# Kernel tuning notes

Measured on AMD Instinct MI355X. Metric: run time of the kernel, lower is better.

Reference implementation:

```python
import jax, jax.numpy as jnp
import numpy as np

B, T, D, H = 8, 1024, 1024, 16
HD = D // H  # 64
FF = 4 * D


def setup_inputs() -> dict:
    key = jax.random.key(0)
    ks = jax.random.split(key, 16)
    s = lambda k, shape, scale: (jax.random.normal(k, shape, dtype=jnp.float32) * scale)
    return {
        "x": s(ks[0], (B, T, D), 1.0),
        "ln1_g": jnp.ones((D,), jnp.float32),
        "ln1_b": jnp.zeros((D,), jnp.float32),
        "ln2_g": jnp.ones((D,), jnp.float32),
        "ln2_b": jnp.zeros((D,), jnp.float32),
        "Wq": s(ks[1], (H, D, HD), 0.02), "bq": jnp.zeros((H, HD), jnp.float32),
        "Wk": s(ks[2], (H, D, HD), 0.02), "bk": jnp.zeros((H, HD), jnp.float32),
        "Wv": s(ks[3], (H, D, HD), 0.02), "bv": jnp.zeros((H, HD), jnp.float32),
        "Wo": s(ks[4], (D, D), 0.02), "bo": jnp.zeros((D,), jnp.float32),
        "W1": s(ks[5], (D, FF), 0.02), "b1": jnp.zeros((FF,), jnp.float32),
        "W2": s(ks[6], (FF, D), 0.02), "b2": jnp.zeros((D,), jnp.float32),
    }


def layer_norm(x, g, b, eps=1e-5):
    mu = jnp.mean(x, axis=-1, keepdims=True)
    var = jnp.mean(jnp.square(x - mu), axis=-1, keepdims=True)
    return (x - mu) * jax.lax.rsqrt(var + eps) * g + b


def reference(x, ln1_g, ln1_b, ln2_g, ln2_b, Wq, bq, Wk, bk, Wv, bv, Wo, bo, W1, b1, W2, b2):
    h = layer_norm(x, ln1_g, ln1_b)
    # Per-head Q/K/V projections, batched over heads (equivalent to the
    # Python loop of per-head Linears in the original module).
    q = jnp.einsum("btd,hde->bhte", h, Wq) + bq[None, :, None, :]
    k = jnp.einsum("btd,hde->bhte", h, Wk) + bk[None, :, None, :]
    v = jnp.einsum("btd,hde->bhte", h, Wv) + bv[None, :, None, :]
    scores = jnp.einsum("bhte,bhse->bhts", q, k) / jnp.sqrt(jnp.float32(HD))
    att = jax.nn.softmax(scores, axis=-1)  # no causal mask in source
    ctx = jnp.einsum("bhts,bhse->bhte", att, v)
    # concat heads along feature dim
    ctx = jnp.transpose(ctx, (0, 2, 1, 3)).reshape(B, T, D)
    attn_out = ctx @ Wo + bo
    x = x + attn_out
    h2 = layer_norm(x, ln2_g, ln2_b)
    ff = jax.nn.gelu(h2 @ W1 + b1, approximate=False) @ W2 + b2
    return x + ff
```

## Files before the change

### kernel.cpp

```cpp
#include <hip/hip_runtime.h>
#include <hip/hip_bf16.h>
#include <cstdint>
#include <cstddef>


typedef __bf16 bf16;
typedef __bf16 bf16x8 __attribute__((ext_vector_type(8)));
typedef __bf16 bf16x4 __attribute__((ext_vector_type(4)));
typedef float  f32x4  __attribute__((ext_vector_type(4)));

#define BB    8
#define TT    1024
#define DD    1024
#define HH    16
#define HDIM  64
#define FFD   4096
#define MROWS (BB*TT)

__device__ __forceinline__ void async_ld16(const void* g, void* l) {
  __builtin_amdgcn_global_load_lds(
      (const __attribute__((address_space(1))) uint32_t*)g,
      (__attribute__((address_space(3))) uint32_t*)l, 16, 0, 0);
}

__global__ void k_transpose_cast(const float* __restrict__ src, bf16* __restrict__ dst,
                                 int K, int N) {
  __shared__ float tile[32][33];
  const size_t boff = (size_t)blockIdx.z * K * N;
  src += boff; dst += boff;
  const int k0 = blockIdx.y * 32, n0 = blockIdx.x * 32;
  const int tx = threadIdx.x, ty = threadIdx.y;
#pragma unroll
  for (int i = 0; i < 4; ++i)
    tile[ty + i*8][tx] = src[(size_t)(k0 + ty + i*8) * N + n0 + tx];
  __syncthreads();
#pragma unroll
  for (int i = 0; i < 4; ++i)
    dst[(size_t)(n0 + ty + i*8) * K + k0 + tx] = (bf16)tile[tx][ty + i*8];
}

__global__ void k_concat_bias(const float* __restrict__ bq, const float* __restrict__ bk,
                              const float* __restrict__ bv, float* __restrict__ out) {
  int i = blockIdx.x * 256 + threadIdx.x;
  float v = (i < 1024) ? bq[i] : (i < 2048) ? bk[i - 1024] : bv[i - 2048];
  out[i] = v;
}

__global__ void k_transpose_v(const bf16* __restrict__ qkv, bf16* __restrict__ vT) {
  __shared__ bf16 tile[32][33];
  const int bh = blockIdx.z;
  const int b = bh >> 4, h = bh & 15;
  const int t0 = blockIdx.x * 32, e0 = blockIdx.y * 32;
  const int tx = threadIdx.x, ty = threadIdx.y;
  const bf16* src = qkv + (size_t)b * TT * 3072 + 2048 + h * 64;
#pragma unroll
  for (int i = 0; i < 4; ++i)
    tile[ty + i*8][tx] = src[(size_t)(t0 + ty + i*8) * 3072 + e0 + tx];
  __syncthreads();
  bf16* dst = vT + ((size_t)bh * 64 + e0) * TT + t0;
#pragma unroll
  for (int i = 0; i < 4; ++i)
    dst[(size_t)(ty + i*8) * TT + tx] = tile[tx][ty + i*8];
}

__global__ void k_layernorm(const float* __restrict__ x, const float* __restrict__ g,
                            const float* __restrict__ b, bf16* __restrict__ out) {
  const int row = blockIdx.x, tid = threadIdx.x;
  const float* xr = x + (size_t)row * DD;
  f32x4 v = *(const f32x4*)(xr + tid * 4);
  float s  = v[0] + v[1] + v[2] + v[3];
  float ss = v[0]*v[0] + v[1]*v[1] + v[2]*v[2] + v[3]*v[3];
#pragma unroll
  for (int m = 1; m < 64; m <<= 1) { s += __shfl_xor(s, m); ss += __shfl_xor(ss, m); }
  __shared__ float red[8];
  const int wid = tid >> 6;
  if ((tid & 63) == 0) { red[wid*2] = s; red[wid*2+1] = ss; }
  __syncthreads();
  s  = red[0] + red[2] + red[4] + red[6];
  ss = red[1] + red[3] + red[5] + red[7];
  const float mu = s * (1.0f / DD);
  const float var = ss * (1.0f / DD) - mu * mu;
  const float rs = rsqrtf(var + 1e-5f);
  bf16x4 o;
#pragma unroll
  for (int j = 0; j < 4; ++j)
    o[j] = (bf16)((v[j] - mu) * rs * g[tid*4 + j] + b[tid*4 + j]);
  *(bf16x4*)&out[(size_t)row * DD + tid * 4] = o;
}

template<int MODE>
__global__ __launch_bounds__(512, 2)
void k_gemm256(const bf16* __restrict__ A, const bf16* __restrict__ Bt,
               const float* __restrict__ bias, bf16* __restrict__ outb,
               int M, int N, int K) {
  __shared__ __align__(16) bf16 As[2][256 * 64];
  __shared__ __align__(16) bf16 Bs[2][256 * 64];
  const int tid = threadIdx.x;
  const int w = tid >> 6, l = tid & 63;
  const int wm = w >> 2, wn = w & 3;
  const int l15 = l & 15, l4 = l >> 4;

  const int nbx = N >> 8;
  const int nwg = gridDim.x;
  const int cpx = nwg >> 3;
  const int swz = (blockIdx.x & 7) * cpx + (blockIdx.x >> 3);
  const int m0 = (swz / nbx) << 8, n0 = (swz % nbx) << 8;

  f32x4 acc[8][4] = {};

  const int srow = l >> 3;
  const int sch = l & 7;

  const int NT = K >> 6;

#define STAGE_A(buf, kt, rb) { \
    const int r_ = (rb) + w*8 + srow; \
    const int ch_ = sch ^ (r_ & 7); \
    async_ld16(A + (size_t)(m0 + r_) * K + (kt)*64 + ch_*8, &As[buf][((rb) + w*8)*64]); }
#define STAGE_B(buf, kt, rb) { \
    const int r_ = (rb) + w*8 + srow; \
    const int ch_ = sch ^ (r_ & 7); \
    async_ld16(Bt + (size_t)(n0 + r_) * K + (kt)*64 + ch_*8, &Bs[buf][((rb) + w*8)*64]); }

  STAGE_A(0, 0, 0)   STAGE_A(0, 0, 64)  STAGE_A(0, 0, 128) STAGE_A(0, 0, 192)
  STAGE_B(0, 0, 0)   STAGE_B(0, 0, 64)  STAGE_B(0, 0, 128) STAGE_B(0, 0, 192)
  STAGE_A(1, 1, 0)   STAGE_A(1, 1, 64)  STAGE_A(1, 1, 128) STAGE_A(1, 1, 192)
  asm volatile("s_waitcnt vmcnt(4)" ::: "memory");
  __builtin_amdgcn_sched_barrier(0);
  __builtin_amdgcn_s_barrier();

  for (int t = 0; t < NT; ++t) {
    const int p = t & 1;
    bf16x8 a0[8], b0[4], a1[8], b1[4];

#pragma unroll
    for (int mf = 0; mf < 8; ++mf) {
      const int row = wm*128 + mf*16 + l15;
      const int ch = l4 ^ (row & 7);
      a0[mf] = *(const bf16x8*)&As[p][row*64 + ch*8];
    }
#pragma unroll
    for (int nf = 0; nf < 4; ++nf) {
      const int row = wn*64 + nf*16 + l15;
      const int ch = l4 ^ (row & 7);
      b0[nf] = *(const bf16x8*)&Bs[p][row*64 + ch*8];
    }
    if (t + 1 < NT) { STAGE_B(p^1, t+1, 0) STAGE_B(p^1, t+1, 64) }
    __builtin_amdgcn_s_barrier();
    asm volatile("s_waitcnt lgkmcnt(0)" ::: "memory");
    __builtin_amdgcn_sched_barrier(0);
    __builtin_amdgcn_s_setprio(1);
#pragma unroll
    for (int mf = 0; mf < 4; ++mf)
#pragma unroll
      for (int nf = 0; nf < 4; ++nf)
        acc[mf][nf] = __builtin_amdgcn_mfma_f32_16x16x32_bf16(a0[mf], b0[nf], acc[mf][nf], 0, 0, 0);
    __builtin_amdgcn_s_setprio(0);
    __builtin_amdgcn_s_barrier();

#pragma unroll
    for (int mf = 0; mf < 8; ++mf) {
      const int row = wm*128 + mf*16 + l15;
      const int ch = (4 + l4) ^ (row & 7);
      a1[mf] = *(const bf16x8*)&As[p][row*64 + ch*8];
    }
#pragma unroll
    for (int nf = 0; nf < 4; ++nf) {
      const int row = wn*64 + nf*16 + l15;
      const int ch = (4 + l4) ^ (row & 7);
      b1[nf] = *(const bf16x8*)&Bs[p][row*64 + ch*8];
    }
    if (t + 1 < NT) { STAGE_B(p^1, t+1, 128) STAGE_B(p^1, t+1, 192) }
    __builtin_amdgcn_s_barrier();
    asm volatile("s_waitcnt lgkmcnt(0)" ::: "memory");
    __builtin_amdgcn_sched_barrier(0);
    __builtin_amdgcn_s_setprio(1);
#pragma unroll
    for (int mf = 4; mf < 8; ++mf)
#pragma unroll
      for (int nf = 0; nf < 4; ++nf)
        acc[mf][nf] = __builtin_amdgcn_mfma_f32_16x16x32_bf16(a0[mf], b0[nf], acc[mf][nf], 0, 0, 0);
    __builtin_amdgcn_s_setprio(0);
    __builtin_amdgcn_s_barrier();

    if (t + 2 < NT) { STAGE_A(p, t+2, 0) STAGE_A(p, t+2, 64) }
    __builtin_amdgcn_s_barrier();
    __builtin_amdgcn_s_setprio(1);
#pragma unroll
    for (int mf = 0; mf < 4; ++mf)
#pragma unroll
      for (int nf = 0; nf < 4; ++nf)
        acc[mf][nf] = __builtin_amdgcn_mfma_f32_16x16x32_bf16(a1[mf], b1[nf], acc[mf][nf], 0, 0, 0);
    __builtin_amdgcn_s_setprio(0);
    __builtin_amdgcn_s_barrier();

    if (t + 2 < NT) { STAGE_A(p, t+2, 128) STAGE_A(p, t+2, 192) }
    __builtin_amdgcn_s_barrier();
    __builtin_amdgcn_s_setprio(1);
#pragma unroll
    for (int mf = 4; mf < 8; ++mf)
#pragma unroll
      for (int nf = 0; nf < 4; ++nf)
        acc[mf][nf] = __builtin_amdgcn_mfma_f32_16x16x32_bf16(a1[mf], b1[nf], acc[mf][nf], 0, 0, 0);
    __builtin_amdgcn_s_setprio(0);
    if (t < NT - 2) { asm volatile("s_waitcnt vmcnt(4)" ::: "memory"); }
    else            { asm volatile("s_waitcnt vmcnt(0)" ::: "memory"); }
    __builtin_amdgcn_sched_barrier(0);
    __builtin_amdgcn_s_barrier();
  }
#undef STAGE_A
#undef STAGE_B

#pragma unroll
  for (int mf = 0; mf < 8; ++mf) {
#pragma unroll
    for (int r = 0; r < 4; ++r) {
      const size_t grow = (size_t)(m0 + wm*128 + mf*16 + l4*4 + r);
      const size_t rowoff = grow * (size_t)N;
#pragma unroll
      for (int nf = 0; nf < 4; ++nf) {
        const int gcol = n0 + wn*64 + nf*16 + l15;
        float v = acc[mf][nf][r] + bias[gcol];
        if constexpr (MODE == 1)
          v = 0.5f * v * (1.0f + erff(v * 0.70710678118654752440f));
        outb[rowoff + gcol] = (bf16)v;
      }
    }
  }
}

template<int MODE>
__global__ __launch_bounds__(256)
void k_gemm(const bf16* __restrict__ A, const bf16* __restrict__ Bt,
            const float* __restrict__ bias, const float* __restrict__ res,
            bf16* __restrict__ outb, float* __restrict__ outf,
            int M, int N, int K) {
  __shared__ __align__(16) bf16 As[128 * 64];
  __shared__ __align__(16) bf16 Bs[128 * 64];
  const int tid = threadIdx.x;
  const int w = tid >> 6, l = tid & 63;
  const int wm = w >> 1, wn = w & 1;
  const int l15 = l & 15, l4 = l >> 4;
  const int m0 = blockIdx.y * 128, n0 = blockIdx.x * 128;

  f32x4 acc[4][4] = {};

  const int srow0 = w * 32 + (l >> 3);
  const int sl7 = l & 7;

  for (int k0 = 0; k0 < K; k0 += 64) {
#pragma unroll
    for (int j = 0; j < 4; ++j) {
      const int row = srow0 + j * 8;
      const int ch = sl7 ^ (row & 7);
      async_ld16(A + (size_t)(m0 + row) * K + k0 + ch * 8, &As[(w*32 + j*8) * 64]);
    }
#pragma unroll
    for (int j = 0; j < 4; ++j) {
      const int row = srow0 + j * 8;
      const int ch = sl7 ^ (row & 7);
      async_ld16(Bt + (size_t)(n0 + row) * K + k0 + ch * 8, &Bs[(w*32 + j*8) * 64]);
    }
    __syncthreads();
#pragma unroll
    for (int kk = 0; kk < 2; ++kk) {
      bf16x8 af[4], bfr[4];
#pragma unroll
      for (int mf = 0; mf < 4; ++mf) {
        const int row = wm*64 + mf*16 + l15;
        const int ch = (kk*4 + l4) ^ (row & 7);
        af[mf] = *(const bf16x8*)&As[row*64 + ch*8];
      }
#pragma unroll
      for (int nf = 0; nf < 4; ++nf) {
        const int row = wn*64 + nf*16 + l15;
        const int ch = (kk*4 + l4) ^ (row & 7);
        bfr[nf] = *(const bf16x8*)&Bs[row*64 + ch*8];
      }
#pragma unroll
      for (int mf = 0; mf < 4; ++mf)
#pragma unroll
        for (int nf = 0; nf < 4; ++nf)
          acc[mf][nf] = __builtin_amdgcn_mfma_f32_16x16x32_bf16(af[mf], bfr[nf], acc[mf][nf], 0, 0, 0);
    }
    __syncthreads();
  }

#pragma unroll
  for (int mf = 0; mf < 4; ++mf) {
#pragma unroll
    for (int r = 0; r < 4; ++r) {
      const size_t grow = (size_t)(m0 + wm*64 + mf*16 + l4*4 + r);
      const size_t rowoff = grow * (size_t)N;
#pragma unroll
      for (int nf = 0; nf < 4; ++nf) {
        const int gcol = n0 + wn*64 + nf*16 + l15;
        float v = acc[mf][nf][r] + bias[gcol];
        if constexpr (MODE == 1)
          v = 0.5f * v * (1.0f + erff(v * 0.70710678118654752440f));
        if constexpr (MODE == 2) {
          v += res[rowoff + gcol];
          outf[rowoff + gcol] = v;
        } else {
          outb[rowoff + gcol] = (bf16)v;
        }
      }
    }
  }
}

__global__ __launch_bounds__(256)
void k_attn(const bf16* __restrict__ qkv, const bf16* __restrict__ vT,
            bf16* __restrict__ ctx) {
  const int qt = blockIdx.x, h = blockIdx.y, b = blockIdx.z;
  const int tid = threadIdx.x;
  const int w = tid >> 6, l = tid & 63;
  const int l15 = l & 15, l4 = l >> 4;

  __shared__ __align__(16) bf16 Ks[2][64 * 64];
  __shared__ __align__(16) bf16 Vs[2][64 * 64];
  __shared__ __align__(16) bf16 P[4][16][72];

  const bf16* base = qkv + (size_t)b * TT * 3072;
  const bf16* Qp = base + h * 64;
  const bf16* Kp = base + 1024 + h * 64;
  const bf16* Vtp = vT + ((size_t)(b * HH + h)) * HDIM * TT;

  const int qrow = qt * 64 + w * 16 + l15;
  bf16x8 qf[2];
  qf[0] = *(const bf16x8*)&Qp[(size_t)qrow * 3072 + l4 * 8];
  qf[1] = *(const bf16x8*)&Qp[(size_t)qrow * 3072 + 32 + l4 * 8];

  f32x4 oacc[4] = {};
  float mrow[4] = {-1e30f, -1e30f, -1e30f, -1e30f};
  float lrow[4] = {0.f, 0.f, 0.f, 0.f};

  const int sr = (l >> 3);
  const int sl7 = l & 7;

  auto stage = [&](int buf, int t) {
    const int kv0 = t * 64;
#pragma unroll
    for (int j = 0; j < 2; ++j) {
      const int row = w*16 + j*8 + sr;
      const int ch = sl7 ^ (row & 7);
      async_ld16(Kp + (size_t)(kv0 + row) * 3072 + ch * 8, &Ks[buf][(w*16 + j*8) * 64]);
    }
#pragma unroll
    for (int j = 0; j < 2; ++j) {
      const int row = w*16 + j*8 + sr;
      const int ch = sl7 ^ (row & 7);
      async_ld16(Vtp + (size_t)row * TT + kv0 + ch * 8, &Vs[buf][(w*16 + j*8) * 64]);
    }
  };

  stage(0, 0);
  for (int t = 0; t < TT / 64; ++t) {
    const int cur = t & 1;
    __syncthreads();
    if (t + 1 < TT / 64) stage(cur ^ 1, t + 1);

    f32x4 sacc[4] = {};
#pragma unroll
    for (int nf = 0; nf < 4; ++nf) {
      const int row = nf*16 + l15;
#pragma unroll
      for (int kk = 0; kk < 2; ++kk) {
        const int ch = (kk*4 + l4) ^ (row & 7);
        bf16x8 kfr = *(const bf16x8*)&Ks[cur][row*64 + ch*8];
        sacc[nf] = __builtin_amdgcn_mfma_f32_16x16x32_bf16(qf[kk], kfr, sacc[nf], 0, 0, 0);
      }
    }
    float mnew[4], ef[4];
#pragma unroll
    for (int r = 0; r < 4; ++r) {
      float mx = -1e30f;
#pragma unroll
      for (int nf = 0; nf < 4; ++nf) { sacc[nf][r] *= 0.125f; mx = fmaxf(mx, sacc[nf][r]); }
      mx = fmaxf(mx, __shfl_xor(mx, 1));
      mx = fmaxf(mx, __shfl_xor(mx, 2));
      mx = fmaxf(mx, __shfl_xor(mx, 4));
      mx = fmaxf(mx, __shfl_xor(mx, 8));
      mnew[r] = fmaxf(mrow[r], mx);
      ef[r] = __expf(mrow[r] - mnew[r]);
      mrow[r] = mnew[r];
    }
#pragma unroll
    for (int r = 0; r < 4; ++r) {
      float rs = 0.f;
#pragma unroll
      for (int nf = 0; nf < 4; ++nf) {
        const float p = __expf(sacc[nf][r] - mnew[r]);
        rs += p;
        P[w][l4*4 + r][l15 + nf*16] = (bf16)p;
      }
      rs += __shfl_xor(rs, 1); rs += __shfl_xor(rs, 2);
      rs += __shfl_xor(rs, 4); rs += __shfl_xor(rs, 8);
      lrow[r] = lrow[r] * ef[r] + rs;
#pragma unroll
      for (int nf = 0; nf < 4; ++nf) oacc[nf][r] *= ef[r];
    }
#pragma unroll
    for (int kk = 0; kk < 2; ++kk) {
      bf16x8 pa = *(const bf16x8*)&P[w][l15][kk*32 + l4*8];
#pragma unroll
      for (int nf = 0; nf < 4; ++nf) {
        const int row = nf*16 + l15;
        const int ch = (kk*4 + l4) ^ (row & 7);
        bf16x8 vb = *(const bf16x8*)&Vs[cur][row*64 + ch*8];
        oacc[nf] = __builtin_amdgcn_mfma_f32_16x16x32_bf16(pa, vb, oacc[nf], 0, 0, 0);
      }
    }
  }
  bf16* outp = ctx + ((size_t)b * TT + qt * 64 + w * 16) * DD + h * 64;
#pragma unroll
  for (int nf = 0; nf < 4; ++nf)
#pragma unroll
    for (int r = 0; r < 4; ++r)
      outp[(size_t)(l4*4 + r) * DD + l15 + nf*16] = (bf16)(oacc[nf][r] / lrow[r]);
}

extern "C" void kernel_launch(void* const* d_in, const int* in_sizes, int n_in,
                              void* d_out, int out_size, void* d_ws, size_t ws_size,
                              hipStream_t stream) {
  const float* x     = (const float*)d_in[0];
  const float* ln1_g = (const float*)d_in[1];
  const float* ln1_b = (const float*)d_in[2];
  const float* ln2_g = (const float*)d_in[3];
  const float* ln2_b = (const float*)d_in[4];
  const float* Wq    = (const float*)d_in[5];
  const float* bq    = (const float*)d_in[6];
  const float* Wk    = (const float*)d_in[7];
  const float* bk    = (const float*)d_in[8];
  const float* Wv    = (const float*)d_in[9];
  const float* bv    = (const float*)d_in[10];
  const float* Wo    = (const float*)d_in[11];
  const float* bo    = (const float*)d_in[12];
  const float* W1    = (const float*)d_in[13];
  const float* b1    = (const float*)d_in[14];
  const float* W2    = (const float*)d_in[15];
  const float* b2    = (const float*)d_in[16];
  float* out = (float*)d_out;

  char* ws = (char*)d_ws;
  bf16* h1    = (bf16*)(ws + 0);
  bf16* vT    = (bf16*)(ws + 0);
  bf16* qkv   = (bf16*)(ws + 16777216);
  bf16* ctx   = (bf16*)(ws + 67108864);
  bf16* u     = (bf16*)(ws + 16777216);
  float* x1   = (float*)(ws + 83886080);
  bf16* wtqkv = (bf16*)(ws + 117440512);
  bf16* wot   = (bf16*)(ws + 123731968);
  bf16* w1t   = (bf16*)(ws + 125829120);
  bf16* w2t   = (bf16*)(ws + 134217728);
  float* bqkv = (float*)(ws + 142606336);
  bf16* h2 = h1;

  dim3 tb(32, 8);
  k_transpose_cast<<<dim3(2, 32, 16), tb, 0, stream>>>(Wq, wtqkv, DD, HDIM);
  k_transpose_cast<<<dim3(2, 32, 16), tb, 0, stream>>>(Wk, wtqkv + 1024*1024, DD, HDIM);
  k_transpose_cast<<<dim3(2, 32, 16), tb, 0, stream>>>(Wv, wtqkv + 2048*1024, DD, HDIM);
  k_transpose_cast<<<dim3(32, 32, 1), tb, 0, stream>>>(Wo, wot, DD, DD);
  k_transpose_cast<<<dim3(128, 32, 1), tb, 0, stream>>>(W1, w1t, DD, FFD);
  k_transpose_cast<<<dim3(32, 128, 1), tb, 0, stream>>>(W2, w2t, FFD, DD);
  k_concat_bias<<<dim3(12), 256, 0, stream>>>(bq, bk, bv, bqkv);

  k_layernorm<<<dim3(MROWS), 256, 0, stream>>>(x, ln1_g, ln1_b, h1);

  k_gemm256<0><<<dim3((MROWS/256)*(3072/256)), 512, 0, stream>>>(
      h1, wtqkv, bqkv, qkv, MROWS, 3072, DD);

  k_transpose_v<<<dim3(32, 2, 128), tb, 0, stream>>>(qkv, vT);

  k_attn<<<dim3(16, 16, 8), 256, 0, stream>>>(qkv, vT, ctx);

  k_gemm<2><<<dim3(8, 64), 256, 0, stream>>>(ctx, wot, bo, x,
                                             nullptr, x1, MROWS, DD, DD);

  k_layernorm<<<dim3(MROWS), 256, 0, stream>>>(x1, ln2_g, ln2_b, h2);

  k_gemm256<1><<<dim3((MROWS/256)*(FFD/256)), 512, 0, stream>>>(
      h2, w1t, b1, u, MROWS, FFD, DD);

  k_gemm<2><<<dim3(8, 64), 256, 0, stream>>>(u, w2t, b2, x1,
                                             nullptr, out, MROWS, DD, FFD);

  (void)in_sizes; (void)n_in; (void)out_size; (void)ws_size;
}
```

Measured before the change: 472.3 us.

## Reschedule GEMM fragment loads and enlarge attention tiles with lazy rescale

The 256-tile GEMM main loop now loads A fragments in four-row halves, which cuts live registers. It also moves all of the second-k-half LDS reads into one phase and issues the A prefetch in a single step, removing two barriers. The attention kernel now runs 8 waves per block over 128 query rows, so each K/V tile staged in LDS is shared by more rows, and it uses an XCD-aware block-id swizzle. It also skips the online-softmax rescale of the accumulators unless the running max grows by more than 8, which adds a wave-wide vote but avoids most of the rescaling work.

```diff
diff --git a/kernel.cpp b/kernel.cpp
--- a/kernel.cpp
+++ b/kernel.cpp
@@ -131,19 +131,17 @@
 
   for (int t = 0; t < NT; ++t) {
     const int p = t & 1;
-    bf16x8 a0[8], b0[4], a1[8], b1[4];
-
-#pragma unroll
-    for (int mf = 0; mf < 8; ++mf) {
-      const int row = wm*128 + mf*16 + l15;
-      const int ch = l4 ^ (row & 7);
-      a0[mf] = *(const bf16x8*)&As[p][row*64 + ch*8];
-    }
+    bf16x8 b0[4], b1[4], af[4], ag[4];
+
 #pragma unroll
     for (int nf = 0; nf < 4; ++nf) {
       const int row = wn*64 + nf*16 + l15;
-      const int ch = l4 ^ (row & 7);
-      b0[nf] = *(const bf16x8*)&Bs[p][row*64 + ch*8];
+      b0[nf] = *(const bf16x8*)&Bs[p][row*64 + (l4 ^ (row & 7))*8];
+    }
+#pragma unroll
+    for (int mf = 0; mf < 4; ++mf) {
+      const int row = wm*128 + mf*16 + l15;
+      af[mf] = *(const bf16x8*)&As[p][row*64 + (l4 ^ (row & 7))*8];
     }
     if (t + 1 < NT) { STAGE_B(p^1, t+1, 0) STAGE_B(p^1, t+1, 64) }
     __builtin_amdgcn_s_barrier();
@@ -154,21 +152,14 @@
     for (int mf = 0; mf < 4; ++mf)
 #pragma unroll
       for (int nf = 0; nf < 4; ++nf)
-        acc[mf][nf] = __builtin_amdgcn_mfma_f32_16x16x32_bf16(a0[mf], b0[nf], acc[mf][nf], 0, 0, 0);
+        acc[mf][nf] = __builtin_amdgcn_mfma_f32_16x16x32_bf16(af[mf], b0[nf], acc[mf][nf], 0, 0, 0);
     __builtin_amdgcn_s_setprio(0);
     __builtin_amdgcn_s_barrier();
 
 #pragma unroll
-    for (int mf = 0; mf < 8; ++mf) {
-      const int row = wm*128 + mf*16 + l15;
-      const int ch = (4 + l4) ^ (row & 7);
-      a1[mf] = *(const bf16x8*)&As[p][row*64 + ch*8];
-    }
-#pragma unroll
-    for (int nf = 0; nf < 4; ++nf) {
-      const int row = wn*64 + nf*16 + l15;
-      const int ch = (4 + l4) ^ (row & 7);
-      b1[nf] = *(const bf16x8*)&Bs[p][row*64 + ch*8];
+    for (int mf = 0; mf < 4; ++mf) {
+      const int row = wm*128 + (mf+4)*16 + l15;
+      ag[mf] = *(const bf16x8*)&As[p][row*64 + (l4 ^ (row & 7))*8];
     }
     if (t + 1 < NT) { STAGE_B(p^1, t+1, 128) STAGE_B(p^1, t+1, 192) }
     __builtin_amdgcn_s_barrier();
@@ -176,32 +167,48 @@
     __builtin_amdgcn_sched_barrier(0);
     __builtin_amdgcn_s_setprio(1);
 #pragma unroll
-    for (int mf = 4; mf < 8; ++mf)
+    for (int mf = 0; mf < 4; ++mf)
 #pragma unroll
       for (int nf = 0; nf < 4; ++nf)
-        acc[mf][nf] = __builtin_amdgcn_mfma_f32_16x16x32_bf16(a0[mf], b0[nf], acc[mf][nf], 0, 0, 0);
+        acc[mf+4][nf] = __builtin_amdgcn_mfma_f32_16x16x32_bf16(ag[mf], b0[nf], acc[mf+4][nf], 0, 0, 0);
     __builtin_amdgcn_s_setprio(0);
     __builtin_amdgcn_s_barrier();
 
-    if (t + 2 < NT) { STAGE_A(p, t+2, 0) STAGE_A(p, t+2, 64) }
-    __builtin_amdgcn_s_barrier();
+#pragma unroll
+    for (int nf = 0; nf < 4; ++nf) {
+      const int row = wn*64 + nf*16 + l15;
+      b1[nf] = *(const bf16x8*)&Bs[p][row*64 + ((4+l4) ^ (row & 7))*8];
+    }
+#pragma unroll
+    for (int mf = 0; mf < 4; ++mf) {
+      const int row = wm*128 + mf*16 + l15;
+      af[mf] = *(const bf16x8*)&As[p][row*64 + ((4+l4) ^ (row & 7))*8];
+    }
+#pragma unroll
+    for (int mf = 0; mf < 4; ++mf) {
+      const int row = wm*128 + (mf+4)*16 + l15;
+      ag[mf] = *(const bf16x8*)&As[p][row*64 + ((4+l4) ^ (row & 7))*8];
+    }
+    __builtin_amdgcn_s_barrier();
+    asm volatile("s_waitcnt lgkmcnt(0)" ::: "memory");
+    __builtin_amdgcn_sched_barrier(0);
     __builtin_amdgcn_s_setprio(1);
 #pragma unroll
     for (int mf = 0; mf < 4; ++mf)
 #pragma unroll
       for (int nf = 0; nf < 4; ++nf)
-        acc[mf][nf] = __builtin_amdgcn_mfma_f32_16x16x32_bf16(a1[mf], b1[nf], acc[mf][nf], 0, 0, 0);
+        acc[mf][nf] = __builtin_amdgcn_mfma_f32_16x16x32_bf16(af[mf], b1[nf], acc[mf][nf], 0, 0, 0);
     __builtin_amdgcn_s_setprio(0);
     __builtin_amdgcn_s_barrier();
 
-    if (t + 2 < NT) { STAGE_A(p, t+2, 128) STAGE_A(p, t+2, 192) }
-    __builtin_amdgcn_s_barrier();
+    if (t + 2 < NT) { STAGE_A(p, t+2, 0) STAGE_A(p, t+2, 64)
+                      STAGE_A(p, t+2, 128) STAGE_A(p, t+2, 192) }
     __builtin_amdgcn_s_setprio(1);
 #pragma unroll
-    for (int mf = 4; mf < 8; ++mf)
+    for (int mf = 0; mf < 4; ++mf)
 #pragma unroll
       for (int nf = 0; nf < 4; ++nf)
-        acc[mf][nf] = __builtin_amdgcn_mfma_f32_16x16x32_bf16(a1[mf], b1[nf], acc[mf][nf], 0, 0, 0);
+        acc[mf+4][nf] = __builtin_amdgcn_mfma_f32_16x16x32_bf16(ag[mf], b1[nf], acc[mf+4][nf], 0, 0, 0);
     __builtin_amdgcn_s_setprio(0);
     if (t < NT - 2) { asm volatile("s_waitcnt vmcnt(4)" ::: "memory"); }
     else            { asm volatile("s_waitcnt vmcnt(0)" ::: "memory"); }
@@ -309,24 +316,28 @@
   }
 }
 
-__global__ __launch_bounds__(256)
+__global__ __launch_bounds__(512)
 void k_attn(const bf16* __restrict__ qkv, const bf16* __restrict__ vT,
             bf16* __restrict__ ctx) {
-  const int qt = blockIdx.x, h = blockIdx.y, b = blockIdx.z;
   const int tid = threadIdx.x;
   const int w = tid >> 6, l = tid & 63;
   const int l15 = l & 15, l4 = l >> 4;
 
+  const int gid = ((int)blockIdx.x & 7) * 128 + ((int)blockIdx.x >> 3);
+  const int qt = gid & 7;
+  const int bh = gid >> 3;
+  const int h = bh & 15, b = bh >> 4;
+
   __shared__ __align__(16) bf16 Ks[2][64 * 64];
   __shared__ __align__(16) bf16 Vs[2][64 * 64];
-  __shared__ __align__(16) bf16 P[4][16][72];
+  __shared__ __align__(16) bf16 P[8][16][72];
 
   const bf16* base = qkv + (size_t)b * TT * 3072;
   const bf16* Qp = base + h * 64;
   const bf16* Kp = base + 1024 + h * 64;
-  const bf16* Vtp = vT + ((size_t)(b * HH + h)) * HDIM * TT;
-
-  const int qrow = qt * 64 + w * 16 + l15;
+  const bf16* Vtp = vT + (size_t)bh * HDIM * TT;
+
+  const int qrow = qt * 128 + w * 16 + l15;
   bf16x8 qf[2];
   qf[0] = *(const bf16x8*)&Qp[(size_t)qrow * 3072 + l4 * 8];
   qf[1] = *(const bf16x8*)&Qp[(size_t)qrow * 3072 + 32 + l4 * 8];
@@ -335,23 +346,13 @@
   float mrow[4] = {-1e30f, -1e30f, -1e30f, -1e30f};
   float lrow[4] = {0.f, 0.f, 0.f, 0.f};
 
-  const int sr = (l >> 3);
-  const int sl7 = l & 7;
+  const int srow = w * 8 + (l >> 3);
+  const int sch = (l & 7) ^ (srow & 7);
 
   auto stage = [&](int buf, int t) {
     const int kv0 = t * 64;
-#pragma unroll
-    for (int j = 0; j < 2; ++j) {
-      const int row = w*16 + j*8 + sr;
-      const int ch = sl7 ^ (row & 7);
-      async_ld16(Kp + (size_t)(kv0 + row) * 3072 + ch * 8, &Ks[buf][(w*16 + j*8) * 64]);
-    }
-#pragma unroll
-    for (int j = 0; j < 2; ++j) {
-      const int row = w*16 + j*8 + sr;
-      const int ch = sl7 ^ (row & 7);
-      async_ld16(Vtp + (size_t)row * TT + kv0 + ch * 8, &Vs[buf][(w*16 + j*8) * 64]);
-    }
+    async_ld16(Kp + (size_t)(kv0 + srow) * 3072 + sch * 8, &Ks[buf][w * 512]);
+    async_ld16(Vtp + (size_t)srow * TT + kv0 + sch * 8, &Vs[buf][w * 512]);
   };
 
   stage(0, 0);
@@ -371,34 +372,43 @@
         sacc[nf] = __builtin_amdgcn_mfma_f32_16x16x32_bf16(qf[kk], kfr, sacc[nf], 0, 0, 0);
       }
     }
-    float mnew[4], ef[4];
+    float mx[4];
+    int ok = 1;
 #pragma unroll
     for (int r = 0; r < 4; ++r) {
-      float mx = -1e30f;
-#pragma unroll
-      for (int nf = 0; nf < 4; ++nf) { sacc[nf][r] *= 0.125f; mx = fmaxf(mx, sacc[nf][r]); }
-      mx = fmaxf(mx, __shfl_xor(mx, 1));
-      mx = fmaxf(mx, __shfl_xor(mx, 2));
-      mx = fmaxf(mx, __shfl_xor(mx, 4));
-      mx = fmaxf(mx, __shfl_xor(mx, 8));
-      mnew[r] = fmaxf(mrow[r], mx);
-      ef[r] = __expf(mrow[r] - mnew[r]);
-      mrow[r] = mnew[r];
+      float m = -1e30f;
+#pragma unroll
+      for (int nf = 0; nf < 4; ++nf) { sacc[nf][r] *= 0.125f; m = fmaxf(m, sacc[nf][r]); }
+      m = fmaxf(m, __shfl_xor(m, 1));
+      m = fmaxf(m, __shfl_xor(m, 2));
+      m = fmaxf(m, __shfl_xor(m, 4));
+      m = fmaxf(m, __shfl_xor(m, 8));
+      mx[r] = m;
+      ok &= (m <= mrow[r] + 8.0f);
+    }
+    if (!__all(ok)) {
+#pragma unroll
+      for (int r = 0; r < 4; ++r) {
+        const float mn = fmaxf(mrow[r], mx[r]);
+        const float e = __expf(mrow[r] - mn);
+        mrow[r] = mn;
+        lrow[r] *= e;
+#pragma unroll
+        for (int nf = 0; nf < 4; ++nf) oacc[nf][r] *= e;
+      }
     }
 #pragma unroll
     for (int r = 0; r < 4; ++r) {
       float rs = 0.f;
 #pragma unroll
       for (int nf = 0; nf < 4; ++nf) {
-        const float p = __expf(sacc[nf][r] - mnew[r]);
-        rs += p;
-        P[w][l4*4 + r][l15 + nf*16] = (bf16)p;
+        const float pv = __expf(sacc[nf][r] - mrow[r]);
+        rs += pv;
+        P[w][l4*4 + r][l15 + nf*16] = (bf16)pv;
       }
       rs += __shfl_xor(rs, 1); rs += __shfl_xor(rs, 2);
       rs += __shfl_xor(rs, 4); rs += __shfl_xor(rs, 8);
-      lrow[r] = lrow[r] * ef[r] + rs;
-#pragma unroll
-      for (int nf = 0; nf < 4; ++nf) oacc[nf][r] *= ef[r];
+      lrow[r] += rs;
     }
 #pragma unroll
     for (int kk = 0; kk < 2; ++kk) {
@@ -412,7 +422,7 @@
       }
     }
   }
-  bf16* outp = ctx + ((size_t)b * TT + qt * 64 + w * 16) * DD + h * 64;
+  bf16* outp = ctx + ((size_t)b * TT + qt * 128 + w * 16) * DD + h * 64;
 #pragma unroll
   for (int nf = 0; nf < 4; ++nf)
 #pragma unroll
@@ -472,7 +482,7 @@
 
   k_transpose_v<<<dim3(32, 2, 128), tb, 0, stream>>>(qkv, vT);
 
-  k_attn<<<dim3(16, 16, 8), 256, 0, stream>>>(qkv, vT, ctx);
+  k_attn<<<dim3(1024), 512, 0, stream>>>(qkv, vT, ctx);
 
   k_gemm<2><<<dim3(8, 64), 256, 0, stream>>>(ctx, wot, bo, x,
                                              nullptr, x1, MROWS, DD, DD);
```

New measurement: 443.8 us. 6.0% less time.
